# Kernel tuning notes

Measured on AMD Instinct MI355X. Metric: run time of the kernel, lower is better.

Reference implementation:

```python
import jax, jax.numpy as jnp
import numpy as np

NEG_SLOPE = 0.01  # torch LeakyReLU default

def setup_inputs() -> dict:
    key = jax.random.key(0)
    ks = jax.random.split(key, 8)
    B, T, D = 8, 2048, 512
    E, H = 8, 2 * D  # n_experts, ffn hidden
    s = 0.02
    return {
        "x":  jax.random.normal(ks[0], (B, T, D), dtype=jnp.float32),
        "Wr": jax.random.normal(ks[1], (D, E), dtype=jnp.float32) * s,
        "br": jnp.zeros((E,), dtype=jnp.float32),
        "W1": jax.random.normal(ks[2], (E, D, H), dtype=jnp.float32) * s,
        "b1": jnp.zeros((E, H), dtype=jnp.float32),
        "W2": jax.random.normal(ks[3], (E, H, D), dtype=jnp.float32) * s,
        "b2": jnp.zeros((E, D), dtype=jnp.float32),
    }

def reference(x, Wr, br, W1, b1, W2, b2):
    B, T, D = x.shape
    E = Wr.shape[1]
    top_k = 2
    balancing_coef = 1e-4
    x_flat = x.reshape(B * T, D)  # [N, D]

    # router: softmax over experts
    router_probs = jax.nn.softmax(x_flat @ Wr + br, axis=-1)  # [N, E]
    top_weights, top_indices = jax.lax.top_k(router_probs, top_k)  # [N, k]

    # dense all-expert FFN (faithful to original: every expert on every token)
    h = jax.nn.leaky_relu(jnp.einsum('nd,edh->neh', x_flat, W1) + b1, NEG_SLOPE)  # [N, E, H]
    expert_out = jax.nn.leaky_relu(jnp.einsum('neh,ehd->ned', h, W2) + b2, NEG_SLOPE)  # [N, E, D]
    # dropout is identity in eval mode

    # gather top-k expert outputs and combine with router weights
    top_out = jnp.take_along_axis(expert_out, top_indices[:, :, None], axis=1)  # [N, k, D]
    out_flat = jnp.sum(top_out * top_weights[:, :, None], axis=1)  # [N, D]
    output = out_flat.reshape(B, T, D)

    # load-balancing loss
    target = jnp.full((E,), 1.0 / E, dtype=x.dtype)
    mean_probs = jnp.mean(router_probs, axis=0)
    gating_loss = jnp.mean((target - mean_probs) ** 2) * balancing_coef
    return (output, gating_loss)
```

## Files before the change

### kernel.cpp

```cpp
#include <hip/hip_runtime.h>
#include <hip/hip_bf16.h>

constexpr int D_    = 512;
constexpr int H_    = 1024;
constexpr int E_    = 8;
constexpr int NTOK_ = 16384;
constexpr int MT_   = 64;
constexpr int NPAIR_= 2*NTOK_;
constexpr float NEG_ = 0.01f;

typedef short s16x8 __attribute__((ext_vector_type(8)));
typedef float f32x4 __attribute__((ext_vector_type(4)));

#define MFMA16(a,b,c) __builtin_amdgcn_mfma_f32_16x16x32_bf16((a),(b),(c),0,0,0)

__device__ __forceinline__ unsigned short f2bf(float f) {
  unsigned u = __float_as_uint(f);
  u += 0x7FFFu + ((u >> 16) & 1u);
  return (unsigned short)(u >> 16);
}
__device__ __forceinline__ float bf2f(unsigned u16) {
  return __uint_as_float(u16 << 16);
}
__device__ __forceinline__ float leaky(float v) {
  return v > 0.f ? v : NEG_ * v;
}

__global__ __launch_bounds__(256) void prep_kernel(
    const float* __restrict__ x, const float* __restrict__ Wr,
    const float* __restrict__ br,
    const float* __restrict__ W1, const float* __restrict__ W2,
    unsigned short* __restrict__ W1s, unsigned short* __restrict__ W2s,
    int* __restrict__ cnt, float* __restrict__ psum,
    int* __restrict__ tokE, int* __restrict__ tokSlot, float* __restrict__ tokW) {
  const int blk = blockIdx.x;
  const int tid = threadIdx.x;
  if (blk < 64) {
    __shared__ int lcnt[E_];
    __shared__ int gbase[E_];
    __shared__ float lp[E_];
    if (tid < E_) { lcnt[tid] = 0; lp[tid] = 0.f; }
    __syncthreads();

    int t = blk * 256 + tid;
    float acc[E_];
#pragma unroll
    for (int e = 0; e < E_; e++) acc[e] = br[e];
    const float4* xr = (const float4*)(x + (size_t)t * D_);
    for (int i = 0; i < D_ / 4; i++) {
      float4 v = xr[i];
      const float* w = Wr + (size_t)i * 4 * E_;
#pragma unroll
      for (int e = 0; e < E_; e++)
        acc[e] += v.x * w[e] + v.y * w[8 + e] + v.z * w[16 + e] + v.w * w[24 + e];
    }
    float mx = acc[0];
#pragma unroll
    for (int e = 1; e < E_; e++) mx = fmaxf(mx, acc[e]);
    float p[E_]; float s = 0.f;
#pragma unroll
    for (int e = 0; e < E_; e++) { p[e] = expf(acc[e] - mx); s += p[e]; }
    float inv = 1.f / s;
#pragma unroll
    for (int e = 0; e < E_; e++) p[e] *= inv;

    float m1 = -1.f, m2 = -1.f; int i1 = 0, i2 = 0;
#pragma unroll
    for (int e = 0; e < E_; e++) {
      float pe = p[e];
      if (pe > m1)      { m2 = m1; i2 = i1; m1 = pe; i1 = e; }
      else if (pe > m2) { m2 = pe; i2 = e; }
    }
    int s1 = atomicAdd(&lcnt[i1], 1);
    int s2 = atomicAdd(&lcnt[i2], 1);

#pragma unroll
    for (int e = 0; e < E_; e++) {
      float v = p[e];
#pragma unroll
      for (int o = 32; o > 0; o >>= 1) v += __shfl_xor(v, o);
      if ((tid & 63) == 0) atomicAdd(&lp[e], v);
    }
    __syncthreads();
    if (tid < E_) {
      gbase[tid] = atomicAdd(&cnt[tid * 16], lcnt[tid]);
      atomicAdd(&psum[tid * 16], lp[tid]);
    }
    __syncthreads();
    tokE[2 * t]     = i1; tokSlot[2 * t]     = gbase[i1] + s1; tokW[2 * t]     = m1;
    tokE[2 * t + 1] = i2; tokSlot[2 * t + 1] = gbase[i2] + s2; tokW[2 * t + 1] = m2;
  } else {
    __shared__ float ldsf[64][68];
    int bid = blk - 64;
    const float* src;
    int e, kt, tc, srcStride;
    bool isW1 = bid < 1024;
    if (isW1) {
      e = bid >> 7; kt = (bid >> 4) & 7; tc = bid & 15; srcStride = 1024;
      src = W1 + ((size_t)(e * 512 + kt * 64)) * 1024 + tc * 64;
    } else {
      int b2 = bid - 1024;
      e = b2 >> 7; kt = (b2 >> 3) & 15; tc = b2 & 7; srcStride = 512;
      src = W2 + ((size_t)(e * 1024 + kt * 64)) * 512 + tc * 64;
    }
#pragma unroll
    for (int rep = 0; rep < 4; rep++) {
      int row = rep * 16 + (tid >> 4);
      int c4  = (tid & 15) * 4;
      float4 v = *(const float4*)(src + (size_t)row * srcStride + c4);
      ldsf[row][c4] = v.x; ldsf[row][c4 + 1] = v.y;
      ldsf[row][c4 + 2] = v.z; ldsf[row][c4 + 3] = v.w;
    }
    __syncthreads();
    int wv = tid >> 6, lane = tid & 63;
#pragma unroll
    for (int qi = 0; qi < 2; qi++) {
      int q = wv * 2 + qi;
      int ks = q >> 2, nt = q & 3;
      int k0 = ks * 32 + (lane >> 4) * 8;
      int n  = nt * 16 + (lane & 15);
      s16x8 v;
#pragma unroll
      for (int j = 0; j < 8; j++) v[j] = (short)f2bf(ldsf[k0 + j][n]);
      if (isW1) {
        int ntg = tc * 4 + nt, kkg = kt * 2 + ks;
        *(s16x8*)(W1s + (((size_t)e << 16) + (ntg << 10) + (kkg << 6) + lane) * 8) = v;
      } else {
        int ntg = tc * 4 + nt, kkg = kt * 2 + ks;
        *(s16x8*)(W2s + (((size_t)e << 16) + (ntg << 11) + (kkg << 6) + lane) * 8) = v;
      }
    }
  }
}

__global__ __launch_bounds__(256) void assign_kernel(
    const int* __restrict__ tokE, const int* __restrict__ tokSlot,
    const int* __restrict__ cnt, const float* __restrict__ psum,
    int* __restrict__ posOfTok, int* __restrict__ tokOfPos,
    float* __restrict__ loss_out) {
  __shared__ int soff[E_];
  int tid = threadIdx.x;
  if (tid == 0) {
    int o = 0;
#pragma unroll
    for (int e = 0; e < E_; e++) { soff[e] = o; o += cnt[e * 16]; }
  }
  __syncthreads();
  int p = blockIdx.x * 256 + tid;
  int pos = soff[tokE[p]] + tokSlot[p];
  posOfTok[p] = pos;
  tokOfPos[pos] = p >> 1;
  if (blockIdx.x == 0 && tid == 0) {
    float l = 0.f;
#pragma unroll
    for (int e = 0; e < E_; e++) {
      float d = 0.125f - psum[e * 16] / (float)NTOK_;
      l += d * d;
    }
    *loss_out = (l / 8.f) * 1e-4f;
  }
}

__global__ __launch_bounds__(512, 2) void ffn_kernel(
    const float* __restrict__ x,
    const unsigned short* __restrict__ W1s, const unsigned short* __restrict__ W2s,
    const float* __restrict__ b1, const float* __restrict__ b2,
    const int* __restrict__ cnt, const int* __restrict__ tokOfPos,
    unsigned short* __restrict__ buf) {
  const int e = blockIdx.x & 7;
  const int tile = blockIdx.x >> 3;
  int nTok = 0, base0 = 0;
#pragma unroll
  for (int i = 0; i < E_; i++) {
    int ci = cnt[i * 16];
    if (i < e) base0 += ci;
    if (i == e) nTok = ci;
  }
  const int start = tile * MT_;
  if (start >= nTok) return;
  const int valid = min(MT_, nTok - start);
  const int base = base0 + start;

  __shared__ __align__(16) unsigned short xs[MT_][D_ + 8];
  __shared__ __align__(16) unsigned short hs[MT_][D_ + 8];

  const int tid = threadIdx.x;
  const int w = tid >> 6;
  const int lane = tid & 63;

  for (int r = w; r < MT_; r += 8) {
    int tok = tokOfPos[base + min(r, valid - 1)];
    const float4* src = (const float4*)(x + (size_t)tok * D_);
    float4 a = src[lane * 2], b = src[lane * 2 + 1];
    s16x8 v;
    v[0] = (short)f2bf(a.x); v[1] = (short)f2bf(a.y);
    v[2] = (short)f2bf(a.z); v[3] = (short)f2bf(a.w);
    v[4] = (short)f2bf(b.x); v[5] = (short)f2bf(b.y);
    v[6] = (short)f2bf(b.z); v[7] = (short)f2bf(b.w);
    *(s16x8*)&xs[r][lane * 8] = v;
  }
  __syncthreads();

  const int qm = lane & 15;
  const int qk = (lane >> 4) * 8;
  const int qr = (lane >> 4) * 4;

  f32x4 acc2[4][4];
#pragma unroll
  for (int mi = 0; mi < 4; mi++)
#pragma unroll
    for (int ni = 0; ni < 4; ni++) acc2[mi][ni] = {0.f, 0.f, 0.f, 0.f};

  const unsigned short* B1w = W1s + ((size_t)(e * 64 + w * 4) * 16) * 512 + lane * 8;
  const unsigned short* B2w = W2s + ((size_t)(e * 32 + w * 4) * 32) * 512 + lane * 8;

  for (int c = 0; c < 2; c++) {
    f32x4 acc1[4][4];
#pragma unroll
    for (int mi = 0; mi < 4; mi++)
#pragma unroll
      for (int ni = 0; ni < 4; ni++) acc1[mi][ni] = {0.f, 0.f, 0.f, 0.f};

    const unsigned short* B1c = B1w + (size_t)(c * 32 * 16) * 512;
    float bb[4];
#pragma unroll
    for (int ni = 0; ni < 4; ni++)
      bb[ni] = b1[e * H_ + c * 512 + w * 64 + ni * 16 + qm];

    s16x8 bfp[2][4], afp[2][4];
#pragma unroll
    for (int s = 0; s < 2; s++) {
#pragma unroll
      for (int ni = 0; ni < 4; ni++)
        bfp[s][ni] = *(const s16x8*)(B1c + (size_t)(ni * 16 + s) * 512);
#pragma unroll
      for (int mi = 0; mi < 4; mi++)
        afp[s][mi] = *(const s16x8*)&xs[mi * 16 + qm][s * 32 + qk];
    }
#pragma unroll
    for (int kk = 0; kk < 16; kk++) {
      s16x8 bcur[4], acur[4];
#pragma unroll
      for (int ni = 0; ni < 4; ni++) bcur[ni] = bfp[kk & 1][ni];
#pragma unroll
      for (int mi = 0; mi < 4; mi++) acur[mi] = afp[kk & 1][mi];
      if (kk + 2 < 16) {
#pragma unroll
        for (int ni = 0; ni < 4; ni++)
          bfp[kk & 1][ni] = *(const s16x8*)(B1c + (size_t)(ni * 16 + kk + 2) * 512);
#pragma unroll
        for (int mi = 0; mi < 4; mi++)
          afp[kk & 1][mi] = *(const s16x8*)&xs[mi * 16 + qm][(kk + 2) * 32 + qk];
      }
#pragma unroll
      for (int ni = 0; ni < 4; ni++)
#pragma unroll
        for (int mi = 0; mi < 4; mi++)
          acc1[mi][ni] = MFMA16(acur[mi], bcur[ni], acc1[mi][ni]);
    }
    __syncthreads();

    const unsigned short* B2c = B2w + (size_t)(c * 16) * 512;
    s16x8 b2p[2][4];
#pragma unroll
    for (int s = 0; s < 2; s++)
#pragma unroll
      for (int ni = 0; ni < 4; ni++)
        b2p[s][ni] = *(const s16x8*)(B2c + (size_t)(ni * 32 + s) * 512);

#pragma unroll
    for (int ni = 0; ni < 4; ni++) {
      int hcol = w * 64 + ni * 16 + qm;
#pragma unroll
      for (int mi = 0; mi < 4; mi++)
#pragma unroll
        for (int r4 = 0; r4 < 4; r4++)
          hs[mi * 16 + qr + r4][hcol] = f2bf(leaky(acc1[mi][ni][r4] + bb[ni]));
    }
    __syncthreads();

    s16x8 a2p[2][4];
#pragma unroll
    for (int s = 0; s < 2; s++)
#pragma unroll
      for (int mi = 0; mi < 4; mi++)
        a2p[s][mi] = *(const s16x8*)&hs[mi * 16 + qm][s * 32 + qk];
#pragma unroll
    for (int kk = 0; kk < 16; kk++) {
      s16x8 bcur[4], acur[4];
#pragma unroll
      for (int ni = 0; ni < 4; ni++) bcur[ni] = b2p[kk & 1][ni];
#pragma unroll
      for (int mi = 0; mi < 4; mi++) acur[mi] = a2p[kk & 1][mi];
      if (kk + 2 < 16) {
#pragma unroll
        for (int ni = 0; ni < 4; ni++)
          b2p[kk & 1][ni] = *(const s16x8*)(B2c + (size_t)(ni * 32 + kk + 2) * 512);
#pragma unroll
        for (int mi = 0; mi < 4; mi++)
          a2p[kk & 1][mi] = *(const s16x8*)&hs[mi * 16 + qm][(kk + 2) * 32 + qk];
      }
#pragma unroll
      for (int ni = 0; ni < 4; ni++)
#pragma unroll
        for (int mi = 0; mi < 4; mi++)
          acc2[mi][ni] = MFMA16(acur[mi], bcur[ni], acc2[mi][ni]);
    }
  }

#pragma unroll
  for (int mi = 0; mi < 4; mi++) {
#pragma unroll
    for (int r4 = 0; r4 < 4; r4++) {
      int row = mi * 16 + qr + r4;
      if (row < valid) {
        size_t rowbase = (size_t)(base + row) * D_;
#pragma unroll
        for (int ni = 0; ni < 4; ni++) {
          int col = w * 64 + ni * 16 + qm;
          float v = leaky(acc2[mi][ni][r4] + b2[e * D_ + col]);
          buf[rowbase + col] = f2bf(v);
        }
      }
    }
  }
}

__global__ __launch_bounds__(256) void combine_kernel(
    const unsigned short* __restrict__ buf, const int* __restrict__ posOfTok,
    const float* __restrict__ tokW, float* __restrict__ out) {
  int t = blockIdx.x * 4 + (threadIdx.x >> 6);
  int lane = threadIdx.x & 63;
  int p0 = posOfTok[2 * t], p1 = posOfTok[2 * t + 1];
  float w0 = tokW[2 * t], w1 = tokW[2 * t + 1];
  uint4 u0 = ((const uint4*)(buf + (size_t)p0 * D_))[lane];
  uint4 u1 = ((const uint4*)(buf + (size_t)p1 * D_))[lane];
  float4 oA, oB;
  oA.x = w0 * bf2f(u0.x & 0xFFFFu) + w1 * bf2f(u1.x & 0xFFFFu);
  oA.y = w0 * bf2f(u0.x >> 16)     + w1 * bf2f(u1.x >> 16);
  oA.z = w0 * bf2f(u0.y & 0xFFFFu) + w1 * bf2f(u1.y & 0xFFFFu);
  oA.w = w0 * bf2f(u0.y >> 16)     + w1 * bf2f(u1.y >> 16);
  oB.x = w0 * bf2f(u0.z & 0xFFFFu) + w1 * bf2f(u1.z & 0xFFFFu);
  oB.y = w0 * bf2f(u0.z >> 16)     + w1 * bf2f(u1.z >> 16);
  oB.z = w0 * bf2f(u0.w & 0xFFFFu) + w1 * bf2f(u1.w & 0xFFFFu);
  oB.w = w0 * bf2f(u0.w >> 16)     + w1 * bf2f(u1.w >> 16);
  float4* dst = (float4*)(out + (size_t)t * D_);
  dst[lane * 2]     = oA;
  dst[lane * 2 + 1] = oB;
}

extern "C" void kernel_launch(void* const* d_in, const int* in_sizes, int n_in,
                              void* d_out, int out_size, void* d_ws, size_t ws_size,
                              hipStream_t stream) {
  const float* x  = (const float*)d_in[0];
  const float* Wr = (const float*)d_in[1];
  const float* br = (const float*)d_in[2];
  const float* W1 = (const float*)d_in[3];
  const float* b1 = (const float*)d_in[4];
  const float* W2 = (const float*)d_in[5];
  const float* b2 = (const float*)d_in[6];
  float* out = (float*)d_out;

  char* ws = (char*)d_ws;
  int*   cnt      = (int*)(ws + 0);
  float* psum     = (float*)(ws + 512);
  int*   tokE     = (int*)(ws + 4096);
  int*   tokSlot  = (int*)(ws + 4096 + 1 * 131072);
  float* tokW     = (float*)(ws + 4096 + 2 * 131072);
  int*   posOfTok = (int*)(ws + 4096 + 3 * 131072);
  int*   tokOfPos = (int*)(ws + 4096 + 4 * 131072);
  unsigned short* W1s = (unsigned short*)(ws + (1u << 20));
  unsigned short* W2s = (unsigned short*)(ws + (1u << 20) + 16777216u);
  unsigned short* buf = (unsigned short*)(ws + (1u << 20) + 33554432u);

  hipMemsetAsync(d_ws, 0, 2048, stream);
  prep_kernel<<<64 + 2048, 256, 0, stream>>>(x, Wr, br, W1, W2, W1s, W2s,
                                             cnt, psum, tokE, tokSlot, tokW);
  assign_kernel<<<NPAIR_ / 256, 256, 0, stream>>>(tokE, tokSlot, cnt, psum,
                                                  posOfTok, tokOfPos,
                                                  out + (size_t)NTOK_ * D_);
  ffn_kernel<<<(NTOK_ / MT_) * E_, 512, 0, stream>>>(x, W1s, W2s, b1, b2,
                                                     cnt, tokOfPos, buf);
  combine_kernel<<<NTOK_ / 4, 256, 0, stream>>>(buf, posOfTok, tokW, out);
}
```

Measured before the change: 295.6 us.

## Restructure expert FFN with 1024-thread blocks and LDS-staged router

The FFN kernel now uses 16 waves per block. All 1024 hidden columns are computed in one pass and written back into a single shared buffer that replaces the separate x and h tiles. The weight operand swaps roles so that weights stream from global as the A operand and tokens come from LDS, and stores become vectorized ushort4. The router part of the prep kernel goes from one thread per token to 64-token tiles staged through LDS, with the reduction split across four waves, which spreads the router work over more blocks. The aim is to remove the two-chunk recomputation loop and improve parallelism, at the cost of larger blocks and a possible drop in occupancy.

```diff
diff --git a/kernel.cpp b/kernel.cpp
--- a/kernel.cpp
+++ b/kernel.cpp
@@ -35,100 +35,123 @@
     int* __restrict__ tokE, int* __restrict__ tokSlot, float* __restrict__ tokW) {
   const int blk = blockIdx.x;
   const int tid = threadIdx.x;
-  if (blk < 64) {
-    __shared__ int lcnt[E_];
-    __shared__ int gbase[E_];
-    __shared__ float lp[E_];
-    if (tid < E_) { lcnt[tid] = 0; lp[tid] = 0.f; }
-    __syncthreads();
-
-    int t = blk * 256 + tid;
+  __shared__ float SH[8256 + 32];
+  if (blk < 256) {
+    const int t0 = blk * 64;
+    float* xt   = SH;
+    float* red  = SH;
+    float* lp   = SH + 8256;
+    int*  lcnt  = (int*)(SH + 8256 + 8);
+    int*  gbase = (int*)(SH + 8256 + 16);
+    if (tid < 8) { lcnt[tid] = 0; lp[tid] = 0.f; }
+
+    const int tq = tid & 63;
+    const int q  = tid >> 6;
     float acc[E_];
 #pragma unroll
-    for (int e = 0; e < E_; e++) acc[e] = br[e];
-    const float4* xr = (const float4*)(x + (size_t)t * D_);
-    for (int i = 0; i < D_ / 4; i++) {
-      float4 v = xr[i];
-      const float* w = Wr + (size_t)i * 4 * E_;
+    for (int e = 0; e < E_; e++) acc[e] = 0.f;
+
+    for (int c = 0; c < 4; c++) {
+      __syncthreads();
+#pragma unroll
+      for (int it = 0; it < 8; it++) {
+        int f = it * 256 + tid;
+        int row = f >> 5, c4 = f & 31;
+        float4 v = *(const float4*)(x + (size_t)(t0 + row) * D_ + c * 128 + c4 * 4);
+        float* d = xt + row * 129 + c4 * 4;
+        d[0] = v.x; d[1] = v.y; d[2] = v.z; d[3] = v.w;
+      }
+      __syncthreads();
+#pragma unroll
+      for (int j = 0; j < 32; j++) {
+        float xv = xt[tq * 129 + q * 32 + j];
+        const float* wr = Wr + (size_t)(c * 128 + q * 32 + j) * E_;
+#pragma unroll
+        for (int e = 0; e < E_; e++) acc[e] += xv * wr[e];
+      }
+    }
+    __syncthreads();
+#pragma unroll
+    for (int e = 0; e < E_; e++) red[(q * 64 + tq) * 8 + e] = acc[e];
+    __syncthreads();
+
+    float m1 = -1.f, m2 = -1.f; int i1 = 0, i2 = 0, s1 = 0, s2 = 0;
+    if (tid < 64) {
+      float p[E_];
 #pragma unroll
       for (int e = 0; e < E_; e++)
-        acc[e] += v.x * w[e] + v.y * w[8 + e] + v.z * w[16 + e] + v.w * w[24 + e];
-    }
-    float mx = acc[0];
-#pragma unroll
-    for (int e = 1; e < E_; e++) mx = fmaxf(mx, acc[e]);
-    float p[E_]; float s = 0.f;
-#pragma unroll
-    for (int e = 0; e < E_; e++) { p[e] = expf(acc[e] - mx); s += p[e]; }
-    float inv = 1.f / s;
-#pragma unroll
-    for (int e = 0; e < E_; e++) p[e] *= inv;
-
-    float m1 = -1.f, m2 = -1.f; int i1 = 0, i2 = 0;
-#pragma unroll
-    for (int e = 0; e < E_; e++) {
-      float pe = p[e];
-      if (pe > m1)      { m2 = m1; i2 = i1; m1 = pe; i1 = e; }
-      else if (pe > m2) { m2 = pe; i2 = e; }
-    }
-    int s1 = atomicAdd(&lcnt[i1], 1);
-    int s2 = atomicAdd(&lcnt[i2], 1);
-
-#pragma unroll
-    for (int e = 0; e < E_; e++) {
-      float v = p[e];
-#pragma unroll
-      for (int o = 32; o > 0; o >>= 1) v += __shfl_xor(v, o);
-      if ((tid & 63) == 0) atomicAdd(&lp[e], v);
-    }
-    __syncthreads();
-    if (tid < E_) {
+        p[e] = br[e] + red[tid * 8 + e] + red[(64 + tid) * 8 + e]
+             + red[(128 + tid) * 8 + e] + red[(192 + tid) * 8 + e];
+      float mx = p[0];
+#pragma unroll
+      for (int e = 1; e < E_; e++) mx = fmaxf(mx, p[e]);
+      float s = 0.f;
+#pragma unroll
+      for (int e = 0; e < E_; e++) { p[e] = expf(p[e] - mx); s += p[e]; }
+      float inv = 1.f / s;
+#pragma unroll
+      for (int e = 0; e < E_; e++) p[e] *= inv;
+
+#pragma unroll
+      for (int e = 0; e < E_; e++) {
+        float pe = p[e];
+        if (pe > m1)      { m2 = m1; i2 = i1; m1 = pe; i1 = e; }
+        else if (pe > m2) { m2 = pe; i2 = e; }
+      }
+      s1 = atomicAdd(&lcnt[i1], 1);
+      s2 = atomicAdd(&lcnt[i2], 1);
+#pragma unroll
+      for (int e = 0; e < E_; e++) atomicAdd(&lp[e], p[e]);
+    }
+    __syncthreads();
+    if (tid < 8) {
       gbase[tid] = atomicAdd(&cnt[tid * 16], lcnt[tid]);
       atomicAdd(&psum[tid * 16], lp[tid]);
     }
     __syncthreads();
-    tokE[2 * t]     = i1; tokSlot[2 * t]     = gbase[i1] + s1; tokW[2 * t]     = m1;
-    tokE[2 * t + 1] = i2; tokSlot[2 * t + 1] = gbase[i2] + s2; tokW[2 * t + 1] = m2;
+    if (tid < 64) {
+      int gt = t0 + tid;
+      tokE[2 * gt]     = i1; tokSlot[2 * gt]     = gbase[i1] + s1; tokW[2 * gt]     = m1;
+      tokE[2 * gt + 1] = i2; tokSlot[2 * gt + 1] = gbase[i2] + s2; tokW[2 * gt + 1] = m2;
+    }
   } else {
-    __shared__ float ldsf[64][68];
-    int bid = blk - 64;
+    float* ldsf = SH;
+    int bid = blk - 256;
     const float* src;
-    int e, kt, tc, srcStride;
+    int eE, kt, tc, srcStride;
     bool isW1 = bid < 1024;
     if (isW1) {
-      e = bid >> 7; kt = (bid >> 4) & 7; tc = bid & 15; srcStride = 1024;
-      src = W1 + ((size_t)(e * 512 + kt * 64)) * 1024 + tc * 64;
+      eE = bid >> 7; kt = (bid >> 4) & 7; tc = bid & 15; srcStride = 1024;
+      src = W1 + ((size_t)(eE * 512 + kt * 64)) * 1024 + tc * 64;
     } else {
-      int b2 = bid - 1024;
-      e = b2 >> 7; kt = (b2 >> 3) & 15; tc = b2 & 7; srcStride = 512;
-      src = W2 + ((size_t)(e * 1024 + kt * 64)) * 512 + tc * 64;
+      int b2i = bid - 1024;
+      eE = b2i >> 7; kt = (b2i >> 3) & 15; tc = b2i & 7; srcStride = 512;
+      src = W2 + ((size_t)(eE * 1024 + kt * 64)) * 512 + tc * 64;
     }
 #pragma unroll
     for (int rep = 0; rep < 4; rep++) {
       int row = rep * 16 + (tid >> 4);
       int c4  = (tid & 15) * 4;
       float4 v = *(const float4*)(src + (size_t)row * srcStride + c4);
-      ldsf[row][c4] = v.x; ldsf[row][c4 + 1] = v.y;
-      ldsf[row][c4 + 2] = v.z; ldsf[row][c4 + 3] = v.w;
+      float* d = ldsf + row * 68 + c4;
+      d[0] = v.x; d[1] = v.y; d[2] = v.z; d[3] = v.w;
     }
     __syncthreads();
     int wv = tid >> 6, lane = tid & 63;
 #pragma unroll
     for (int qi = 0; qi < 2; qi++) {
-      int q = wv * 2 + qi;
-      int ks = q >> 2, nt = q & 3;
+      int qq = wv * 2 + qi;
+      int ks = qq >> 2, nt = qq & 3;
       int k0 = ks * 32 + (lane >> 4) * 8;
       int n  = nt * 16 + (lane & 15);
       s16x8 v;
 #pragma unroll
-      for (int j = 0; j < 8; j++) v[j] = (short)f2bf(ldsf[k0 + j][n]);
-      if (isW1) {
-        int ntg = tc * 4 + nt, kkg = kt * 2 + ks;
-        *(s16x8*)(W1s + (((size_t)e << 16) + (ntg << 10) + (kkg << 6) + lane) * 8) = v;
-      } else {
-        int ntg = tc * 4 + nt, kkg = kt * 2 + ks;
-        *(s16x8*)(W2s + (((size_t)e << 16) + (ntg << 11) + (kkg << 6) + lane) * 8) = v;
-      }
+      for (int j = 0; j < 8; j++) v[j] = (short)f2bf(ldsf[(k0 + j) * 68 + n]);
+      int ntg = tc * 4 + nt, kkg = kt * 2 + ks;
+      if (isW1)
+        *(s16x8*)(W1s + (((size_t)eE << 16) + (ntg << 10) + (kkg << 6) + lane) * 8) = v;
+      else
+        *(s16x8*)(W2s + (((size_t)eE << 16) + (ntg << 11) + (kkg << 6) + lane) * 8) = v;
     }
   }
 }
@@ -161,7 +184,7 @@
   }
 }
 
-__global__ __launch_bounds__(512, 2) void ffn_kernel(
+__global__ __launch_bounds__(1024, 4) void ffn_kernel(
     const float* __restrict__ x,
     const unsigned short* __restrict__ W1s, const unsigned short* __restrict__ W2s,
     const float* __restrict__ b1, const float* __restrict__ b2,
@@ -181,14 +204,13 @@
   const int valid = min(MT_, nTok - start);
   const int base = base0 + start;
 
-  __shared__ __align__(16) unsigned short xs[MT_][D_ + 8];
-  __shared__ __align__(16) unsigned short hs[MT_][D_ + 8];
+  __shared__ __align__(16) unsigned short L[MT_][1032];
 
   const int tid = threadIdx.x;
   const int w = tid >> 6;
   const int lane = tid & 63;
 
-  for (int r = w; r < MT_; r += 8) {
+  for (int r = w; r < MT_; r += 16) {
     int tok = tokOfPos[base + min(r, valid - 1)];
     const float4* src = (const float4*)(x + (size_t)tok * D_);
     float4 a = src[lane * 2], b = src[lane * 2 + 1];
@@ -197,7 +219,7 @@
     v[2] = (short)f2bf(a.z); v[3] = (short)f2bf(a.w);
     v[4] = (short)f2bf(b.x); v[5] = (short)f2bf(b.y);
     v[6] = (short)f2bf(b.z); v[7] = (short)f2bf(b.w);
-    *(s16x8*)&xs[r][lane * 8] = v;
+    *(s16x8*)&L[r][lane * 8] = v;
   }
   __syncthreads();
 
@@ -205,122 +227,104 @@
   const int qk = (lane >> 4) * 8;
   const int qr = (lane >> 4) * 4;
 
-  f32x4 acc2[4][4];
+  const unsigned short* A1 =
+      W1s + (((size_t)e << 16) + ((size_t)(w * 4) << 10) + lane) * 8;
+  f32x4 acc1[4][4];
 #pragma unroll
   for (int mi = 0; mi < 4; mi++)
 #pragma unroll
+    for (int ni = 0; ni < 4; ni++) acc1[mi][ni] = {0.f, 0.f, 0.f, 0.f};
+
+  s16x8 a1p[2][4];
+#pragma unroll
+  for (int s = 0; s < 2; s++)
+#pragma unroll
+    for (int mi = 0; mi < 4; mi++)
+      a1p[s][mi] = *(const s16x8*)(A1 + (size_t)mi * 8192 + s * 512);
+
+#pragma unroll
+  for (int kk = 0; kk < 16; kk++) {
+    s16x8 bcur[4];
+#pragma unroll
+    for (int ni = 0; ni < 4; ni++)
+      bcur[ni] = *(const s16x8*)&L[ni * 16 + qm][kk * 32 + qk];
+#pragma unroll
+    for (int mi = 0; mi < 4; mi++)
+#pragma unroll
+      for (int ni = 0; ni < 4; ni++)
+        acc1[mi][ni] = MFMA16(a1p[kk & 1][mi], bcur[ni], acc1[mi][ni]);
+    if (kk + 2 < 16) {
+#pragma unroll
+      for (int mi = 0; mi < 4; mi++)
+        a1p[kk & 1][mi] = *(const s16x8*)(A1 + (size_t)mi * 8192 + (kk + 2) * 512);
+    }
+  }
+  __syncthreads();
+
+#pragma unroll
+  for (int mi = 0; mi < 4; mi++) {
+    int hb = w * 64 + mi * 16 + qr;
+    float4 bv = *(const float4*)(b1 + (size_t)e * H_ + hb);
+#pragma unroll
+    for (int ni = 0; ni < 4; ni++) {
+      int tr = ni * 16 + qm;
+      ushort4 pk;
+      pk.x = f2bf(leaky(acc1[mi][ni][0] + bv.x));
+      pk.y = f2bf(leaky(acc1[mi][ni][1] + bv.y));
+      pk.z = f2bf(leaky(acc1[mi][ni][2] + bv.z));
+      pk.w = f2bf(leaky(acc1[mi][ni][3] + bv.w));
+      *(ushort4*)&L[tr][hb] = pk;
+    }
+  }
+  __syncthreads();
+
+  const unsigned short* A2 =
+      W2s + (((size_t)e << 16) + ((size_t)(w * 2) << 11) + lane) * 8;
+  f32x4 acc2[2][4];
+#pragma unroll
+  for (int mi = 0; mi < 2; mi++)
+#pragma unroll
     for (int ni = 0; ni < 4; ni++) acc2[mi][ni] = {0.f, 0.f, 0.f, 0.f};
 
-  const unsigned short* B1w = W1s + ((size_t)(e * 64 + w * 4) * 16) * 512 + lane * 8;
-  const unsigned short* B2w = W2s + ((size_t)(e * 32 + w * 4) * 32) * 512 + lane * 8;
-
-  for (int c = 0; c < 2; c++) {
-    f32x4 acc1[4][4];
-#pragma unroll
-    for (int mi = 0; mi < 4; mi++)
-#pragma unroll
-      for (int ni = 0; ni < 4; ni++) acc1[mi][ni] = {0.f, 0.f, 0.f, 0.f};
-
-    const unsigned short* B1c = B1w + (size_t)(c * 32 * 16) * 512;
-    float bb[4];
+  s16x8 a2p[2][2];
+#pragma unroll
+  for (int s = 0; s < 2; s++)
+#pragma unroll
+    for (int mi = 0; mi < 2; mi++)
+      a2p[s][mi] = *(const s16x8*)(A2 + (size_t)mi * 16384 + s * 512);
+
+#pragma unroll
+  for (int kk = 0; kk < 32; kk++) {
+    s16x8 bcur[4];
 #pragma unroll
     for (int ni = 0; ni < 4; ni++)
-      bb[ni] = b1[e * H_ + c * 512 + w * 64 + ni * 16 + qm];
-
-    s16x8 bfp[2][4], afp[2][4];
-#pragma unroll
-    for (int s = 0; s < 2; s++) {
+      bcur[ni] = *(const s16x8*)&L[ni * 16 + qm][kk * 32 + qk];
+#pragma unroll
+    for (int mi = 0; mi < 2; mi++)
 #pragma unroll
       for (int ni = 0; ni < 4; ni++)
-        bfp[s][ni] = *(const s16x8*)(B1c + (size_t)(ni * 16 + s) * 512);
-#pragma unroll
-      for (int mi = 0; mi < 4; mi++)
-        afp[s][mi] = *(const s16x8*)&xs[mi * 16 + qm][s * 32 + qk];
-    }
-#pragma unroll
-    for (int kk = 0; kk < 16; kk++) {
-      s16x8 bcur[4], acur[4];
-#pragma unroll
-      for (int ni = 0; ni < 4; ni++) bcur[ni] = bfp[kk & 1][ni];
-#pragma unroll
-      for (int mi = 0; mi < 4; mi++) acur[mi] = afp[kk & 1][mi];
-      if (kk + 2 < 16) {
-#pragma unroll
-        for (int ni = 0; ni < 4; ni++)
-          bfp[kk & 1][ni] = *(const s16x8*)(B1c + (size_t)(ni * 16 + kk + 2) * 512);
-#pragma unroll
-        for (int mi = 0; mi < 4; mi++)
-          afp[kk & 1][mi] = *(const s16x8*)&xs[mi * 16 + qm][(kk + 2) * 32 + qk];
-      }
-#pragma unroll
-      for (int ni = 0; ni < 4; ni++)
-#pragma unroll
-        for (int mi = 0; mi < 4; mi++)
-          acc1[mi][ni] = MFMA16(acur[mi], bcur[ni], acc1[mi][ni]);
-    }
-    __syncthreads();
-
-    const unsigned short* B2c = B2w + (size_t)(c * 16) * 512;
-    s16x8 b2p[2][4];
-#pragma unroll
-    for (int s = 0; s < 2; s++)
-#pragma unroll
-      for (int ni = 0; ni < 4; ni++)
-        b2p[s][ni] = *(const s16x8*)(B2c + (size_t)(ni * 32 + s) * 512);
-
+        acc2[mi][ni] = MFMA16(a2p[kk & 1][mi], bcur[ni], acc2[mi][ni]);
+    if (kk + 2 < 32) {
+#pragma unroll
+      for (int mi = 0; mi < 2; mi++)
+        a2p[kk & 1][mi] = *(const s16x8*)(A2 + (size_t)mi * 16384 + (kk + 2) * 512);
+    }
+  }
+
+#pragma unroll
+  for (int mi = 0; mi < 2; mi++) {
+    int ob = w * 32 + mi * 16 + qr;
+    float4 bv = *(const float4*)(b2 + (size_t)e * D_ + ob);
 #pragma unroll
     for (int ni = 0; ni < 4; ni++) {
-      int hcol = w * 64 + ni * 16 + qm;
-#pragma unroll
-      for (int mi = 0; mi < 4; mi++)
-#pragma unroll
-        for (int r4 = 0; r4 < 4; r4++)
-          hs[mi * 16 + qr + r4][hcol] = f2bf(leaky(acc1[mi][ni][r4] + bb[ni]));
-    }
-    __syncthreads();
-
-    s16x8 a2p[2][4];
-#pragma unroll
-    for (int s = 0; s < 2; s++)
-#pragma unroll
-      for (int mi = 0; mi < 4; mi++)
-        a2p[s][mi] = *(const s16x8*)&hs[mi * 16 + qm][s * 32 + qk];
-#pragma unroll
-    for (int kk = 0; kk < 16; kk++) {
-      s16x8 bcur[4], acur[4];
-#pragma unroll
-      for (int ni = 0; ni < 4; ni++) bcur[ni] = b2p[kk & 1][ni];
-#pragma unroll
-      for (int mi = 0; mi < 4; mi++) acur[mi] = a2p[kk & 1][mi];
-      if (kk + 2 < 16) {
-#pragma unroll
-        for (int ni = 0; ni < 4; ni++)
-          b2p[kk & 1][ni] = *(const s16x8*)(B2c + (size_t)(ni * 32 + kk + 2) * 512);
-#pragma unroll
-        for (int mi = 0; mi < 4; mi++)
-          a2p[kk & 1][mi] = *(const s16x8*)&hs[mi * 16 + qm][(kk + 2) * 32 + qk];
-      }
-#pragma unroll
-      for (int ni = 0; ni < 4; ni++)
-#pragma unroll
-        for (int mi = 0; mi < 4; mi++)
-          acc2[mi][ni] = MFMA16(acur[mi], bcur[ni], acc2[mi][ni]);
-    }
-  }
-
-#pragma unroll
-  for (int mi = 0; mi < 4; mi++) {
-#pragma unroll
-    for (int r4 = 0; r4 < 4; r4++) {
-      int row = mi * 16 + qr + r4;
-      if (row < valid) {
-        size_t rowbase = (size_t)(base + row) * D_;
-#pragma unroll
-        for (int ni = 0; ni < 4; ni++) {
-          int col = w * 64 + ni * 16 + qm;
-          float v = leaky(acc2[mi][ni][r4] + b2[e * D_ + col]);
-          buf[rowbase + col] = f2bf(v);
-        }
+      int tok = ni * 16 + qm;
+      if (tok < valid) {
+        ushort4 pk;
+        pk.x = f2bf(leaky(acc2[mi][ni][0] + bv.x));
+        pk.y = f2bf(leaky(acc2[mi][ni][1] + bv.y));
+        pk.z = f2bf(leaky(acc2[mi][ni][2] + bv.z));
+        pk.w = f2bf(leaky(acc2[mi][ni][3] + bv.w));
+        *(ushort4*)(buf + (size_t)(base + tok) * D_ + ob) = pk;
       }
     }
   }
@@ -374,12 +378,12 @@
   unsigned short* buf = (unsigned short*)(ws + (1u << 20) + 33554432u);
 
   hipMemsetAsync(d_ws, 0, 2048, stream);
-  prep_kernel<<<64 + 2048, 256, 0, stream>>>(x, Wr, br, W1, W2, W1s, W2s,
-                                             cnt, psum, tokE, tokSlot, tokW);
+  prep_kernel<<<256 + 2048, 256, 0, stream>>>(x, Wr, br, W1, W2, W1s, W2s,
+                                              cnt, psum, tokE, tokSlot, tokW);
   assign_kernel<<<NPAIR_ / 256, 256, 0, stream>>>(tokE, tokSlot, cnt, psum,
                                                   posOfTok, tokOfPos,
                                                   out + (size_t)NTOK_ * D_);
-  ffn_kernel<<<(NTOK_ / MT_) * E_, 512, 0, stream>>>(x, W1s, W2s, b1, b2,
-                                                     cnt, tokOfPos, buf);
+  ffn_kernel<<<(NTOK_ / MT_) * E_, 1024, 0, stream>>>(x, W1s, W2s, b1, b2,
+                                                      cnt, tokOfPos, buf);
   combine_kernel<<<NTOK_ / 4, 256, 0, stream>>>(buf, posOfTok, tokW, out);
 }
```

Measured after the change: 279.4 us. -5.5%, faster.
